# Kernel optimization log

Measured on AMD Instinct MI355X. Metric: run time of the kernel, lower is better.

The kernel has to match this reference:

```python
import jax, jax.numpy as jnp
import numpy as np
import math

B, S, D, H = 2, 2048, 1024, 16
HD = D // H  # head_dim = 64
NEG = -1.0e9


def _xavier(key, shape, gain):
    fan_in, fan_out = shape[1], shape[0]
    bound = gain * math.sqrt(6.0 / (fan_in + fan_out))
    return jax.random.uniform(key, shape, jnp.float32, -bound, bound)


def setup_inputs() -> dict:
    key = jax.random.key(0)
    ks = jax.random.split(key, 7)
    gain = 1.0 / math.sqrt(2.0)
    q = jax.random.normal(ks[0], (B, S, D), jnp.float32)
    pad_mask = jax.random.randint(ks[1], (B, S), 0, 2) > 0  # True = masked key
    # ensure not all keys masked per row
    pad_mask = pad_mask.at[:, 0].set(False)
    Wq = _xavier(ks[2], (D, D), gain)
    Wk = _xavier(ks[3], (D, D), gain)
    Wv = _xavier(ks[4], (D, D), gain)
    Wo = _xavier(ks[5], (D, D), gain)
    bk = jax.random.normal(ks[6], (4, D), jnp.float32) * 0.02
    return {"q": q, "pad_mask": pad_mask,
            "Wq": Wq, "bq": bk[0], "Wk": Wk, "bk": bk[1],
            "Wv": Wv, "bv": bk[2], "Wo": Wo, "bo": bk[3]}


def reference(q, pad_mask, Wq, bq, Wk, bk, Wv, bv, Wo, bo):
    # Self-attention: k = v = q (k, v args are None in this config)
    x = q
    # torch Linear: y = x @ W.T + b
    qh = (x @ Wq.T + bq).reshape(B, S, H, HD).transpose(0, 2, 1, 3)  # [B,H,S,HD]
    kh = (x @ Wk.T + bk).reshape(B, S, H, HD).transpose(0, 2, 1, 3)
    vh = (x @ Wv.T + bv).reshape(B, S, H, HD).transpose(0, 2, 1, 3)

    scores = jnp.einsum('bhqd,bhkd->bhqk', qh, kh) / math.sqrt(HD)  # [B,H,S,S]
    causal = jnp.triu(jnp.ones((S, S), bool), k=1)                  # [S,S]
    scores = jnp.where(causal[None, None], NEG, scores)
    scores = jnp.where(pad_mask[:, None, None, :], NEG, scores)

    probs = jax.nn.softmax(scores, axis=-1)
    out = jnp.einsum('bhqk,bhkd->bhqd', probs, vh)                  # [B,H,S,HD]
    out = out.transpose(0, 2, 1, 3).reshape(B, S, D)
    return out @ Wo.T + bo
```

## Files before the change

kernel.cpp:

```cpp
#include <hip/hip_runtime.h>
#include <hip/hip_bf16.h>

#define BB 2
#define SS 2048
#define DD 1024
#define HH 16
#define HD 64
#define MM (BB * SS)
#define NQKV 3072

typedef __attribute__((ext_vector_type(8))) short short8;
typedef __attribute__((ext_vector_type(4))) short s16x4;
typedef __attribute__((ext_vector_type(4))) float floatx4;
typedef __attribute__((ext_vector_type(4))) float f32x4;
using bf16 = __hip_bfloat16;

__device__ __forceinline__ float b2f(bf16 x) { return __bfloat162float(x); }
__device__ __forceinline__ short f2bs(float x) {
    bf16 h = __float2bfloat16(x);
    return *reinterpret_cast<short*>(&h);
}
__device__ __forceinline__ float bs2f(short s) {
    bf16 h; *reinterpret_cast<short*>(&h) = s; return __bfloat162float(h);
}

__device__ __forceinline__ int lds_off(int row, int chunk) {
    return row * 64 + ((chunk ^ (row & 7)) * 8);
}

#define GL16(gp, lp)                                                        \
    __builtin_amdgcn_global_load_lds(                                       \
        (const __attribute__((address_space(1))) void*)(gp),                \
        (__attribute__((address_space(3))) void*)(lp), 16, 0, 0)

__global__ __launch_bounds__(256) void convert_wcat(
    const float* __restrict__ Wq, const float* __restrict__ Wk,
    const float* __restrict__ Wv, short* __restrict__ dst)
{
    const int stride = gridDim.x * blockDim.x;
    for (int i = blockIdx.x * blockDim.x + threadIdx.x; i < NQKV * DD / 4; i += stride) {
        const int elem = i * 4;
        const int z    = elem >> 20;
        const int off  = elem & 0xFFFFF;
        const float* src = (z == 0) ? Wq : (z == 1) ? Wk : Wv;
        f32x4 v = *(const f32x4*)(src + off);
        s16x4 o; o[0] = f2bs(v[0]); o[1] = f2bs(v[1]); o[2] = f2bs(v[2]); o[3] = f2bs(v[3]);
        *(s16x4*)(dst + elem) = o;
    }
}

__global__ __launch_bounds__(256) void convert_w(
    const float* __restrict__ W, short* __restrict__ dst)
{
    const int stride = gridDim.x * blockDim.x;
    for (int i = blockIdx.x * blockDim.x + threadIdx.x; i < DD * DD / 4; i += stride) {
        f32x4 v = *(const f32x4*)(W + i * 4);
        s16x4 o; o[0] = f2bs(v[0]); o[1] = f2bs(v[1]); o[2] = f2bs(v[2]); o[3] = f2bs(v[3]);
        *(s16x4*)(dst + i * 4) = o;
    }
}

__global__ __launch_bounds__(256) void convert_x(
    const float* __restrict__ X, short* __restrict__ dst)
{
    const int stride = gridDim.x * blockDim.x;
    for (int i = blockIdx.x * blockDim.x + threadIdx.x; i < MM * DD / 4; i += stride) {
        f32x4 v = *(const f32x4*)(X + i * 4);
        s16x4 o; o[0] = f2bs(v[0]); o[1] = f2bs(v[1]); o[2] = f2bs(v[2]); o[3] = f2bs(v[3]);
        *(s16x4*)(dst + i * 4) = o;
    }
}

__global__ __launch_bounds__(256) void qkv_gemm2(
    const short* __restrict__ Xb, const short* __restrict__ Wcat,
    const float* __restrict__ bq, const float* __restrict__ bk, const float* __restrict__ bv,
    bf16* __restrict__ outQ, bf16* __restrict__ outK, bf16* __restrict__ outV)
{
    __shared__ short As[128 * 64];
    __shared__ short Bs[128 * 64];

    const int tid  = threadIdx.x;
    const int lane = tid & 63;
    const int wave = tid >> 6;
    const int wm   = wave & 1;
    const int wn   = wave >> 1;
    const int g    = lane >> 4;
    const int fr   = lane & 15;

    const int m0 = blockIdx.x * 128;
    const int n0 = blockIdx.y * 128;

    const int srow = wave * 32 + (lane >> 3);
    const int schk = (lane & 7) ^ (lane >> 3);
    const short* agl = Xb   + (size_t)(m0 + srow) * DD + schk * 8;
    const short* bgl = Wcat + (size_t)(n0 + srow) * DD + schk * 8;
    short* alds = &As[wave * 32 * 64];
    short* blds = &Bs[wave * 32 * 64];

    floatx4 acc[4][4];
#pragma unroll
    for (int i = 0; i < 4; ++i)
#pragma unroll
        for (int j = 0; j < 4; ++j) acc[i][j] = (floatx4){0.f, 0.f, 0.f, 0.f};

    for (int kb = 0; kb < DD; kb += 64) {
        __syncthreads();
#pragma unroll
        for (int j = 0; j < 4; ++j) {
            GL16(agl + kb + j * 8 * DD, alds + j * 8 * 64);
            GL16(bgl + kb + j * 8 * DD, blds + j * 8 * 64);
        }
        __syncthreads();

#pragma unroll
        for (int kk = 0; kk < 2; ++kk) {
            const int kc = kk * 4 + g;
            short8 af[4], bf[4];
#pragma unroll
            for (int t = 0; t < 4; ++t) {
                af[t] = *(const short8*)&As[lds_off(wm * 64 + t * 16 + fr, kc)];
                bf[t] = *(const short8*)&Bs[lds_off(wn * 64 + t * 16 + fr, kc)];
            }
#pragma unroll
            for (int mt = 0; mt < 4; ++mt)
#pragma unroll
                for (int nt = 0; nt < 4; ++nt)
                    acc[mt][nt] = __builtin_amdgcn_mfma_f32_16x16x32_bf16(
                        af[mt], bf[nt], acc[mt][nt], 0, 0, 0);
        }
    }

#pragma unroll
    for (int nt = 0; nt < 4; ++nt) {
        const int n  = n0 + wn * 64 + nt * 16 + fr;
        const int z  = n >> 10;
        const int nn = n & 1023;
        const int h_ = nn >> 6;
        const int d_ = nn & 63;
        const float biasv = ((z == 0) ? bq : (z == 1) ? bk : bv)[nn];
        bf16* outp = (z == 0) ? outQ : (z == 1) ? outK : outV;
#pragma unroll
        for (int mt = 0; mt < 4; ++mt) {
#pragma unroll
            for (int reg = 0; reg < 4; ++reg) {
                const int m  = m0 + wm * 64 + mt * 16 + g * 4 + reg;
                const int b_ = m >> 11;
                const int s_ = m & (SS - 1);
                const float v = acc[mt][nt][reg] + biasv;
                size_t off;
                if (z == 2) off = ((size_t)((b_ * HH + h_) * HD + d_)) * SS + s_;
                else        off = ((size_t)((b_ * HH + h_) * SS + s_)) * HD + d_;
                outp[off] = __float2bfloat16(v);
            }
        }
    }
}

__global__ __launch_bounds__(256) void o_gemm2(
    const short* __restrict__ A, const short* __restrict__ Wob,
    const float* __restrict__ bias, float* __restrict__ out)
{
    __shared__ short As[128 * 64];
    __shared__ short Bs[128 * 64];

    const int tid  = threadIdx.x;
    const int lane = tid & 63;
    const int wave = tid >> 6;
    const int wm   = wave & 1;
    const int wn   = wave >> 1;
    const int g    = lane >> 4;
    const int fr   = lane & 15;

    const int m0 = blockIdx.x * 128;
    const int n0 = blockIdx.y * 128;

    const int srow = wave * 32 + (lane >> 3);
    const int schk = (lane & 7) ^ (lane >> 3);
    const short* agl = A   + (size_t)(m0 + srow) * DD + schk * 8;
    const short* bgl = Wob + (size_t)(n0 + srow) * DD + schk * 8;
    short* alds = &As[wave * 32 * 64];
    short* blds = &Bs[wave * 32 * 64];

    floatx4 acc[4][4];
#pragma unroll
    for (int i = 0; i < 4; ++i)
#pragma unroll
        for (int j = 0; j < 4; ++j) acc[i][j] = (floatx4){0.f, 0.f, 0.f, 0.f};

    for (int kb = 0; kb < DD; kb += 64) {
        __syncthreads();
#pragma unroll
        for (int j = 0; j < 4; ++j) {
            GL16(agl + kb + j * 8 * DD, alds + j * 8 * 64);
            GL16(bgl + kb + j * 8 * DD, blds + j * 8 * 64);
        }
        __syncthreads();

#pragma unroll
        for (int kk = 0; kk < 2; ++kk) {
            const int kc = kk * 4 + g;
            short8 af[4], bf[4];
#pragma unroll
            for (int t = 0; t < 4; ++t) {
                af[t] = *(const short8*)&As[lds_off(wm * 64 + t * 16 + fr, kc)];
                bf[t] = *(const short8*)&Bs[lds_off(wn * 64 + t * 16 + fr, kc)];
            }
#pragma unroll
            for (int mt = 0; mt < 4; ++mt)
#pragma unroll
                for (int nt = 0; nt < 4; ++nt)
                    acc[mt][nt] = __builtin_amdgcn_mfma_f32_16x16x32_bf16(
                        af[mt], bf[nt], acc[mt][nt], 0, 0, 0);
        }
    }

#pragma unroll
    for (int nt = 0; nt < 4; ++nt) {
        const int n = n0 + wn * 64 + nt * 16 + fr;
        const float biasv = bias[n];
#pragma unroll
        for (int mt = 0; mt < 4; ++mt) {
#pragma unroll
            for (int reg = 0; reg < 4; ++reg) {
                const int m = m0 + wm * 64 + mt * 16 + g * 4 + reg;
                out[(size_t)m * DD + n] = acc[mt][nt][reg] + biasv;
            }
        }
    }
}

__global__ __launch_bounds__(256) void flash_mfma5(
    const bf16* __restrict__ Qh,
    const bf16* __restrict__ Kh,
    const bf16* __restrict__ VT,
    const int*  __restrict__ pad,
    bf16* __restrict__ attn)
{
    __shared__ short Ks[64 * 64];
    __shared__ short Vs[64 * 64];
    __shared__ short Pld[4][16 * 64];

    const int tid  = threadIdx.x;
    const int lane = tid & 63;
    const int wave = tid >> 6;
    const int xcd = blockIdx.x & 7;
    const int idx = blockIdx.x >> 3;
    const int bh  = (xcd << 2) | (idx & 3);
    const int qt  = 31 - (idx >> 2);
    const int q0  = qt * 64 + wave * 16;
    const int b_  = bh >> 4;
    const int h_  = bh & 15;

    const int g  = lane >> 4;
    const int fr = lane & 15;
    const int k8 = g * 8;

    short* myP = Pld[wave];

    const bf16* qbase = Qh + ((size_t)bh * SS + q0 + fr) * HD + k8;
    short8 qf[2];
#pragma unroll
    for (int hh = 0; hh < 2; ++hh) {
        short8 rawq = *(const short8*)((const short*)qbase + hh * 32);
#pragma unroll
        for (int j = 0; j < 8; ++j) qf[hh][j] = f2bs(bs2f(rawq[j]) * 0.125f);
    }

    const int* padrow = pad + b_ * SS;
    const short* kbh = (const short*)(Kh + (size_t)bh * SS * HD);
    const short* vbh = (const short*)(VT + (size_t)bh * HD * SS);

    const int sr = tid >> 2;
    const int cp = (tid & 3) * 2;

    floatx4 o[4] = {{0,0,0,0},{0,0,0,0},{0,0,0,0},{0,0,0,0}};
    float l_acc[4] = {0.f, 0.f, 0.f, 0.f};

    const int kend = qt * 64 + 63;
    for (int kb = 0; kb <= kend; kb += 64) {
        __syncthreads();
        {
            const short* gk = kbh + (size_t)(kb + sr) * HD + cp * 8;
            *(short8*)&Ks[lds_off(sr, cp)]     = *(const short8*)gk;
            *(short8*)&Ks[lds_off(sr, cp + 1)] = *(const short8*)(gk + 8);
            const short* gv = vbh + (size_t)sr * SS + kb + cp * 8;
            *(short8*)&Vs[lds_off(sr, cp)]     = *(const short8*)gv;
            *(short8*)&Vs[lds_off(sr, cp + 1)] = *(const short8*)(gv + 8);
        }
        __syncthreads();

        floatx4 c[4];
#pragma unroll
        for (int t = 0; t < 4; ++t) {
            short8 kf0 = *(const short8*)&Ks[(t * 16 + fr) * 64 + ((g       ^ (fr & 7)) << 3)];
            short8 kf1 = *(const short8*)&Ks[(t * 16 + fr) * 64 + (((g + 4) ^ (fr & 7)) << 3)];
            floatx4 cc = {0, 0, 0, 0};
            cc = __builtin_amdgcn_mfma_f32_16x16x32_bf16(qf[0], kf0, cc, 0, 0, 0);
            cc = __builtin_amdgcn_mfma_f32_16x16x32_bf16(qf[1], kf1, cc, 0, 0, 0);
            c[t] = cc;
        }

        bool pm[4];
#pragma unroll
        for (int t = 0; t < 4; ++t) pm[t] = (padrow[kb + t * 16 + fr] != 0);

#pragma unroll
        for (int reg = 0; reg < 4; ++reg) {
            const int q   = q0 + g * 4 + reg;
            const int row = g * 4 + reg;
#pragma unroll
            for (int t = 0; t < 4; ++t) {
                const int key = kb + t * 16 + fr;
                const float p = (key <= q && !pm[t]) ? __expf(c[t][reg]) : 0.f;
                l_acc[reg] += p;
                const int col = t * 16 + fr;
                myP[row * 64 + (((col >> 3) ^ (row & 7)) << 3) + (col & 7)] = f2bs(p);
            }
        }

        short8 pf0 = *(const short8*)&myP[fr * 64 + ((g       ^ (fr & 7)) << 3)];
        short8 pf1 = *(const short8*)&myP[fr * 64 + (((g + 4) ^ (fr & 7)) << 3)];
#pragma unroll
        for (int n = 0; n < 4; ++n) {
            short8 vf0 = *(const short8*)&Vs[(n * 16 + fr) * 64 + ((g       ^ (fr & 7)) << 3)];
            short8 vf1 = *(const short8*)&Vs[(n * 16 + fr) * 64 + (((g + 4) ^ (fr & 7)) << 3)];
            o[n] = __builtin_amdgcn_mfma_f32_16x16x32_bf16(pf0, vf0, o[n], 0, 0, 0);
            o[n] = __builtin_amdgcn_mfma_f32_16x16x32_bf16(pf1, vf1, o[n], 0, 0, 0);
        }
    }

    float inv[4];
#pragma unroll
    for (int reg = 0; reg < 4; ++reg) {
        float l = l_acc[reg];
#pragma unroll
        for (int off = 1; off < 16; off <<= 1) l += __shfl_xor(l, off);
        inv[reg] = 1.f / fmaxf(l, 1e-38f);
    }
#pragma unroll
    for (int n = 0; n < 4; ++n) {
#pragma unroll
        for (int reg = 0; reg < 4; ++reg) {
            const int q = q0 + g * 4 + reg;
            attn[((size_t)(b_ * SS + q)) * DD + h_ * HD + n * 16 + fr] =
                __float2bfloat16(o[n][reg] * inv[reg]);
        }
    }
}

extern "C" void kernel_launch(void* const* d_in, const int* in_sizes, int n_in,
                              void* d_out, int out_size, void* d_ws, size_t ws_size,
                              hipStream_t stream) {
    const float* x   = (const float*)d_in[0];
    const int*   pad = (const int*)  d_in[1];
    const float* Wq  = (const float*)d_in[2];
    const float* bq  = (const float*)d_in[3];
    const float* Wk  = (const float*)d_in[4];
    const float* bk  = (const float*)d_in[5];
    const float* Wv  = (const float*)d_in[6];
    const float* bv  = (const float*)d_in[7];
    const float* Wo  = (const float*)d_in[8];
    const float* bo  = (const float*)d_in[9];
    float* out = (float*)d_out;

    const size_t NELEM = (size_t)BB * HH * SS * HD;
    bf16* Qh   = (bf16*)d_ws;
    bf16* Kh   = Qh + NELEM;
    bf16* VT   = Kh + NELEM;
    bf16* attn = VT + NELEM;
    short* Wcat = (short*)d_out;
    short* Xb   = (short*)d_out + (size_t)NQKV * DD;
    short* Wob  = (short*)Qh;

    convert_wcat<<<768, 256, 0, stream>>>(Wq, Wk, Wv, Wcat);
    convert_x<<<1024, 256, 0, stream>>>(x, Xb);

    dim3 gq(MM / 128, NQKV / 128);
    qkv_gemm2<<<gq, 256, 0, stream>>>(Xb, Wcat, bq, bk, bv, Qh, Kh, VT);

    flash_mfma5<<<BB * HH * 32, 256, 0, stream>>>(Qh, Kh, VT, pad, attn);

    convert_w<<<512, 256, 0, stream>>>(Wo, Wob);

    dim3 go(MM / 128, DD / 128);
    o_gemm2<<<go, 256, 0, stream>>>((const short*)attn, Wob, bo, out);
}
```

Measured before the change: 209.0 us.

## Rewrite QKV GEMM as 256x256 8-wave ping-pong pipelined kernel

Replaces the 128x128 single-buffered QKV GEMM with a 256x256 tile kernel that uses 8 waves, double-buffered LDS (128KB dynamic shared memory) and eight sub-phases per iteration. Each phase interleaves global-to-LDS staging of the next K tile with MFMA work on the current one, using raw barriers, vmcnt waits and setprio. Block indices are swizzled so neighbouring blocks share tiles and get better L2 reuse. The aim is to hide memory latency and cut redundant global loads, at the cost of a small grid of 192 blocks and heavy register and LDS use.

```diff
diff --git a/kernel.cpp b/kernel.cpp
--- a/kernel.cpp
+++ b/kernel.cpp
@@ -71,68 +71,122 @@
     }
 }
 
-__global__ __launch_bounds__(256) void qkv_gemm2(
+template <int D, int MH, int NH, class Stage, class Tail>
+__device__ __forceinline__ void phase8(
+    const short* As, const short* Bs, int wm, int wn, int fr, int g,
+    floatx4 (&acc)[8][4], Stage&& stage, Tail&& tail)
+{
+    short8 af[4][2], bfq[2][2];
+    const short* Ad = As + D * (256 * 64);
+    const short* Bd = Bs + D * (256 * 64);
+#pragma unroll
+    for (int t = 0; t < 4; ++t)
+#pragma unroll
+        for (int kk = 0; kk < 2; ++kk)
+            af[t][kk] = *(const short8*)&Ad[lds_off(MH * 128 + wm * 64 + t * 16 + fr, kk * 4 + g)];
+#pragma unroll
+    for (int u = 0; u < 2; ++u)
+#pragma unroll
+        for (int kk = 0; kk < 2; ++kk)
+            bfq[u][kk] = *(const short8*)&Bd[lds_off(NH * 128 + wn * 32 + u * 16 + fr, kk * 4 + g)];
+    stage();
+    __builtin_amdgcn_s_barrier();
+    asm volatile("s_waitcnt lgkmcnt(0)" ::: "memory");
+    __builtin_amdgcn_s_setprio(1);
+#pragma unroll
+    for (int t = 0; t < 4; ++t)
+#pragma unroll
+        for (int u = 0; u < 2; ++u) {
+            acc[MH * 4 + t][NH * 2 + u] = __builtin_amdgcn_mfma_f32_16x16x32_bf16(
+                af[t][0], bfq[u][0], acc[MH * 4 + t][NH * 2 + u], 0, 0, 0);
+            acc[MH * 4 + t][NH * 2 + u] = __builtin_amdgcn_mfma_f32_16x16x32_bf16(
+                af[t][1], bfq[u][1], acc[MH * 4 + t][NH * 2 + u], 0, 0, 0);
+        }
+    __builtin_amdgcn_s_setprio(0);
+    tail();
+    __builtin_amdgcn_s_barrier();
+}
+
+__global__ __launch_bounds__(512, 2) void qkv_gemm8(
     const short* __restrict__ Xb, const short* __restrict__ Wcat,
     const float* __restrict__ bq, const float* __restrict__ bk, const float* __restrict__ bv,
     bf16* __restrict__ outQ, bf16* __restrict__ outK, bf16* __restrict__ outV)
 {
-    __shared__ short As[128 * 64];
-    __shared__ short Bs[128 * 64];
+    extern __shared__ short lds[];
+    short* As = lds;
+    short* Bs = lds + 2 * 256 * 64;
 
     const int tid  = threadIdx.x;
     const int lane = tid & 63;
     const int wave = tid >> 6;
-    const int wm   = wave & 1;
-    const int wn   = wave >> 1;
+    const int wm   = wave >> 2;
+    const int wn   = wave & 3;
     const int g    = lane >> 4;
     const int fr   = lane & 15;
 
-    const int m0 = blockIdx.x * 128;
-    const int n0 = blockIdx.y * 128;
-
-    const int srow = wave * 32 + (lane >> 3);
-    const int schk = (lane & 7) ^ (lane >> 3);
-    const short* agl = Xb   + (size_t)(m0 + srow) * DD + schk * 8;
-    const short* bgl = Wcat + (size_t)(n0 + srow) * DD + schk * 8;
-    short* alds = &As[wave * 32 * 64];
-    short* blds = &Bs[wave * 32 * 64];
-
-    floatx4 acc[4][4];
-#pragma unroll
-    for (int i = 0; i < 4; ++i)
+    const int sw = (blockIdx.x & 7) * 24 + (blockIdx.x >> 3);
+    const int m0 = (sw % 16) * 256;
+    const int n0 = (sw / 16) * 256;
+
+    const int srow8 = lane >> 3;
+    const int schk  = (lane & 7) ^ srow8;
+
+    auto stageA = [&](int d, int h, int kt) {
+#pragma unroll
+        for (int j = 0; j < 2; ++j) {
+            const int r = h * 128 + wave * 16 + j * 8;
+            const short* src = Xb + (size_t)(m0 + r + srow8) * DD + kt * 64 + schk * 8;
+            GL16(src, As + d * (256 * 64) + r * 64);
+        }
+    };
+    auto stageB = [&](int d, int h, int kt) {
+#pragma unroll
+        for (int j = 0; j < 2; ++j) {
+            const int r = h * 128 + wave * 16 + j * 8;
+            const short* src = Wcat + (size_t)(n0 + r + srow8) * DD + kt * 64 + schk * 8;
+            GL16(src, Bs + d * (256 * 64) + r * 64);
+        }
+    };
+
+    floatx4 acc[8][4];
+#pragma unroll
+    for (int i = 0; i < 8; ++i)
 #pragma unroll
         for (int j = 0; j < 4; ++j) acc[i][j] = (floatx4){0.f, 0.f, 0.f, 0.f};
 
-    for (int kb = 0; kb < DD; kb += 64) {
-        __syncthreads();
-#pragma unroll
-        for (int j = 0; j < 4; ++j) {
-            GL16(agl + kb + j * 8 * DD, alds + j * 8 * 64);
-            GL16(bgl + kb + j * 8 * DD, blds + j * 8 * 64);
-        }
-        __syncthreads();
-
-#pragma unroll
-        for (int kk = 0; kk < 2; ++kk) {
-            const int kc = kk * 4 + g;
-            short8 af[4], bf[4];
-#pragma unroll
-            for (int t = 0; t < 4; ++t) {
-                af[t] = *(const short8*)&As[lds_off(wm * 64 + t * 16 + fr, kc)];
-                bf[t] = *(const short8*)&Bs[lds_off(wn * 64 + t * 16 + fr, kc)];
-            }
-#pragma unroll
-            for (int mt = 0; mt < 4; ++mt)
-#pragma unroll
-                for (int nt = 0; nt < 4; ++nt)
-                    acc[mt][nt] = __builtin_amdgcn_mfma_f32_16x16x32_bf16(
-                        af[mt], bf[nt], acc[mt][nt], 0, 0, 0);
-        }
+    stageA(0, 0, 0); stageA(0, 1, 0); stageB(0, 0, 0); stageB(0, 1, 0);
+    stageA(1, 0, 1); stageA(1, 1, 1); stageB(1, 0, 1); stageB(1, 1, 1);
+    asm volatile("s_waitcnt vmcnt(0)" ::: "memory");
+    __builtin_amdgcn_s_barrier();
+
+    auto nop = [] {};
+    auto vm4 = [] { asm volatile("s_waitcnt vmcnt(4)" ::: "memory"); };
+
+    for (int it = 0; it < 8; ++it) {
+        const int t1 = (2 * it + 1) & 15;
+        const int s2 = (2 * it + 2) & 15;
+        const int s3 = (2 * it + 3) & 15;
+        phase8<0, 0, 0>(As, Bs, wm, wn, fr, g, acc,
+                        [&] { if (it) stageA(1, 1, t1); }, nop);
+        phase8<0, 0, 1>(As, Bs, wm, wn, fr, g, acc,
+                        [&] { if (it) stageB(1, 1, t1); }, nop);
+        phase8<0, 1, 0>(As, Bs, wm, wn, fr, g, acc,
+                        [&] { stageA(0, 0, s2); }, nop);
+        phase8<0, 1, 1>(As, Bs, wm, wn, fr, g, acc,
+                        [&] { stageB(0, 0, s2); }, vm4);
+        phase8<1, 0, 0>(As, Bs, wm, wn, fr, g, acc,
+                        [&] { stageA(0, 1, s2); }, nop);
+        phase8<1, 0, 1>(As, Bs, wm, wn, fr, g, acc,
+                        [&] { stageB(0, 1, s2); }, nop);
+        phase8<1, 1, 0>(As, Bs, wm, wn, fr, g, acc,
+                        [&] { stageA(1, 0, s3); }, nop);
+        phase8<1, 1, 1>(As, Bs, wm, wn, fr, g, acc,
+                        [&] { stageB(1, 0, s3); }, vm4);
     }
 
 #pragma unroll
     for (int nt = 0; nt < 4; ++nt) {
-        const int n  = n0 + wn * 64 + nt * 16 + fr;
+        const int n  = n0 + (nt >> 1) * 128 + wn * 32 + (nt & 1) * 16 + fr;
         const int z  = n >> 10;
         const int nn = n & 1023;
         const int h_ = nn >> 6;
@@ -140,10 +194,10 @@
         const float biasv = ((z == 0) ? bq : (z == 1) ? bk : bv)[nn];
         bf16* outp = (z == 0) ? outQ : (z == 1) ? outK : outV;
 #pragma unroll
-        for (int mt = 0; mt < 4; ++mt) {
+        for (int mt = 0; mt < 8; ++mt) {
 #pragma unroll
             for (int reg = 0; reg < 4; ++reg) {
-                const int m  = m0 + wm * 64 + mt * 16 + g * 4 + reg;
+                const int m  = m0 + (mt >> 2) * 128 + wm * 64 + (mt & 3) * 16 + g * 4 + reg;
                 const int b_ = m >> 11;
                 const int s_ = m & (SS - 1);
                 const float v = acc[mt][nt][reg] + biasv;
@@ -372,11 +426,17 @@
     short* Xb   = (short*)d_out + (size_t)NQKV * DD;
     short* Wob  = (short*)Qh;
 
+    static bool qkv8_init = false;
+    if (!qkv8_init) {
+        hipFuncSetAttribute(reinterpret_cast<const void*>(qkv_gemm8),
+                            hipFuncAttributeMaxDynamicSharedMemorySize, 131072);
+        qkv8_init = true;
+    }
+
     convert_wcat<<<768, 256, 0, stream>>>(Wq, Wk, Wv, Wcat);
     convert_x<<<1024, 256, 0, stream>>>(x, Xb);
 
-    dim3 gq(MM / 128, NQKV / 128);
-    qkv_gemm2<<<gq, 256, 0, stream>>>(Xb, Wcat, bq, bk, bv, Qh, Kh, VT);
+    qkv_gemm8<<<192, 512, 131072, stream>>>(Xb, Wcat, bq, bk, bv, Qh, Kh, VT);
 
     flash_mfma5<<<BB * HH * 32, 256, 0, stream>>>(Qh, Kh, VT, pad, attn);
 
```

New measurement: 227.5 us. 8.8% more time.
